# Kernel tuning notes

Measured on AMD Instinct MI355X. Metric: run time of the kernel, lower is better.

The kernel has to match this reference:

```python
import jax, jax.numpy as jnp
import numpy as np
import math

B, S, H = 2, 2048, 2048
NH, NKV, HD = 16, 4, 128


def _rope_tables(seq_len, head_dim):
    # Standard RoPE: freqs over half dim, duplicated to full head_dim.
    inv_freq = 1.0 / (10000.0 ** (np.arange(0, head_dim, 2, dtype=np.float32) / head_dim))
    t = np.arange(seq_len, dtype=np.float32)
    freqs = np.outer(t, inv_freq)  # [S, HD/2]
    emb = np.concatenate([freqs, freqs], axis=-1)  # [S, HD]
    return jnp.asarray(np.cos(emb)), jnp.asarray(np.sin(emb))


def setup_inputs() -> dict:
    key = jax.random.key(0)
    k1, k2, k3, k4 = jax.random.split(key, 4)
    cos, sin = _rope_tables(S, HD)
    return {
        "x": jax.random.normal(k1, (B, S, H), dtype=jnp.float32),
        "cos": cos,
        "sin": sin,
        "Wq": jax.random.normal(k2, (H, NH * HD), dtype=jnp.float32) * (1.0 / math.sqrt(H)),
        "Wkv": jax.random.normal(k3, (H, 2 * NKV * HD), dtype=jnp.float32) * (1.0 / math.sqrt(H)),
        "Wo": jax.random.normal(k4, (NH * HD, H), dtype=jnp.float32) * (1.0 / math.sqrt(NH * HD)),
    }


def _rotate_half(x):
    x1, x2 = jnp.split(x, 2, axis=-1)
    return jnp.concatenate([-x2, x1], axis=-1)


def _apply_rotary(x, cos, sin):
    # x: [B, S, nheads, HD]; cos/sin: [S, HD]
    c = cos[None, :, None, :]
    s = sin[None, :, None, :]
    return x * c + _rotate_half(x) * s


def reference(x, cos, sin, Wq, Wkv, Wo):
    b, s, _ = x.shape
    q = (x @ Wq).reshape(b, s, NH, HD)
    kv = x @ Wkv
    k, v = jnp.split(kv, [NKV * HD], axis=-1)
    k = k.reshape(b, s, NKV, HD)
    v = v.reshape(b, s, NKV, HD)
    q = _apply_rotary(q, cos, sin)
    k = _apply_rotary(k, cos, sin)
    # to [B, heads, S, HD]
    q = jnp.transpose(q, (0, 2, 1, 3))
    k = jnp.transpose(k, (0, 2, 1, 3))
    v = jnp.transpose(v, (0, 2, 1, 3))
    # GQA: repeat K/V heads
    rep = NH // NKV
    k = jnp.repeat(k, rep, axis=1)
    v = jnp.repeat(v, rep, axis=1)
    scale = jnp.asarray(1.0 / math.sqrt(HD), dtype=x.dtype)
    scores = jnp.einsum('bhqd,bhkd->bhqk', q * scale, k)  # [B, NH, S, S]
    causal = jnp.tril(jnp.ones((s, s), dtype=jnp.bool_))
    scores = jnp.where(causal, scores, jnp.asarray(-jnp.inf, scores.dtype))
    attn = jax.nn.softmax(scores, axis=-1)
    out = jnp.einsum('bhqk,bhkd->bhqd', attn, v)
    out = jnp.transpose(out, (0, 2, 1, 3)).reshape(b, s, NH * HD)
    return out @ Wo
```

## Files before the change

kernel.cpp:

```cpp
#include <hip/hip_runtime.h>
#include <math.h>

#define NB 2
#define SEQ 2048
#define HDIM 2048
#define NHD 16
#define NKVH 4
#define HEADD 128
#define MROWS (NB*SEQ)
#define NQCOLS (NHD*HEADD)
#define QKVCOLS 3072

typedef unsigned short ushortT;
typedef __attribute__((ext_vector_type(8))) short short8;
typedef __attribute__((ext_vector_type(4))) float floatx4;
typedef __attribute__((ext_vector_type(4))) unsigned short ushort4v;

__device__ __forceinline__ ushortT f2bf(float f) {
  union { float f; unsigned int u; } v; v.f = f;
  unsigned int r = v.u + 0x7FFFu + ((v.u >> 16) & 1u);
  return (ushortT)(r >> 16);
}
__device__ __forceinline__ float bf2f(ushortT u) {
  union { unsigned int u; float f; } v; v.u = ((unsigned int)u) << 16;
  return v.f;
}

__device__ __forceinline__ unsigned int cvt_pk_bf16(float lo, float hi) {
  unsigned int r;
  asm("v_cvt_pk_bf16_f32 %0, %1, %2" : "=v"(r) : "v"(lo), "v"(hi));
  return r;
}

__device__ __forceinline__ void gload16(const ushortT* g, ushortT* l) {
  __builtin_amdgcn_global_load_lds(
      (const __attribute__((address_space(1))) void*)g,
      (__attribute__((address_space(3))) void*)l, 16, 0, 0);
}

__global__ __launch_bounds__(256) void cast_bf16_kernel(
    const float* __restrict__ in, ushortT* __restrict__ out, int n4) {
  int i = blockIdx.x * 256 + threadIdx.x;
  if (i >= n4) return;
  float4 v = ((const float4*)in)[i];
  ushort4v o;
  o.x = f2bf(v.x); o.y = f2bf(v.y); o.z = f2bf(v.z); o.w = f2bf(v.w);
  ((ushort4v*)out)[i] = o;
}

__global__ __launch_bounds__(256) void transpose_cast_kernel(
    const float* __restrict__ in, ushortT* __restrict__ out, int R, int C) {
  __shared__ ushortT tile[32][33];
  int c0 = blockIdx.x * 32, r0 = blockIdx.y * 32;
  int tx = threadIdx.x & 31, ty = threadIdx.x >> 5;
#pragma unroll
  for (int i = 0; i < 4; ++i)
    tile[ty + i*8][tx] = f2bf(in[(size_t)(r0 + ty + i*8) * C + c0 + tx]);
  __syncthreads();
#pragma unroll
  for (int i = 0; i < 4; ++i)
    out[(size_t)(c0 + ty + i*8) * R + r0 + tx] = tile[tx][ty + i*8];
}

__global__ __launch_bounds__(256) void gemm_bt_kernel(
    const ushortT* __restrict__ A, const ushortT* __restrict__ Bt,
    void* __restrict__ C, int M, int N, int K, int c_fp32) {
  __shared__ __align__(16) ushortT lA[128 * 64];
  __shared__ __align__(16) ushortT lB[128 * 64];
  const int m0 = blockIdx.y * 128;
  const int n0 = blockIdx.x * 128;
  const int tid = threadIdx.x;
  const int wave = tid >> 6, lane = tid & 63;
  const int g = lane >> 4, l15 = lane & 15;
  const int wm = (wave >> 1) * 64, wn = (wave & 1) * 64;
  const int sw = l15 & 7;

  floatx4 acc[4][4] = {};

  for (int kt = 0; kt < K; kt += 64) {
    __syncthreads();
#pragma unroll
    for (int i = 0; i < 4; ++i) {
      int s = i * 256 + tid;
      int r = s >> 3, j = s & 7;
      int col8 = j ^ (r & 7);
      gload16(A  + (size_t)(m0 + r) * K + kt + col8 * 8, lA + s * 8);
      gload16(Bt + (size_t)(n0 + r) * K + kt + col8 * 8, lB + s * 8);
    }
    __syncthreads();
#pragma unroll
    for (int ks = 0; ks < 2; ++ks) {
      short8 af[4], bfv[4];
#pragma unroll
      for (int t = 0; t < 4; ++t) {
        af[t]  = *(const short8*)(lA + (wm + t * 16 + l15) * 64 + ((ks * 4 + g) ^ sw) * 8);
        bfv[t] = *(const short8*)(lB + (wn + t * 16 + l15) * 64 + ((ks * 4 + g) ^ sw) * 8);
      }
#pragma unroll
      for (int mt = 0; mt < 4; ++mt)
#pragma unroll
        for (int nt = 0; nt < 4; ++nt)
          acc[mt][nt] = __builtin_amdgcn_mfma_f32_16x16x32_bf16(
              af[mt], bfv[nt], acc[mt][nt], 0, 0, 0);
    }
  }

#pragma unroll
  for (int mt = 0; mt < 4; ++mt)
#pragma unroll
    for (int nt = 0; nt < 4; ++nt)
#pragma unroll
      for (int r = 0; r < 4; ++r) {
        int row = m0 + wm + mt * 16 + g * 4 + r;
        int col = n0 + wn + nt * 16 + l15;
        float v = acc[mt][nt][r];
        if (c_fp32) ((float*)C)[(size_t)row * N + col] = v;
        else ((ushortT*)C)[(size_t)row * N + col] = f2bf(v);
      }
}

__global__ __launch_bounds__(256) void rope_q_kernel(
    const ushortT* __restrict__ QKVtmp, const float* __restrict__ cosT,
    const float* __restrict__ sinT, ushortT* __restrict__ Qr) {
  int idx = blockIdx.x * 256 + threadIdx.x;
  int d = idx & 63;
  int t = idx >> 6;
  int h = t & (NHD - 1);
  int bs = t >> 4;
  int s = bs & (SEQ - 1);
  int b = bs >> 11;
  float c = cosT[s * HEADD + d], sn = sinT[s * HEADD + d];
  float q1 = bf2f(QKVtmp[(size_t)bs * QKVCOLS + h * HEADD + d]);
  float q2 = bf2f(QKVtmp[(size_t)bs * QKVCOLS + h * HEADD + d + 64]);
  size_t o = ((size_t)(b * NHD + h) * SEQ + s) * HEADD + d;
  Qr[o]      = f2bf(q1 * c - q2 * sn);
  Qr[o + 64] = f2bf(q2 * c + q1 * sn);
}

__global__ __launch_bounds__(256) void rope_k_kernel(
    const ushortT* __restrict__ QKVtmp, const float* __restrict__ cosT,
    const float* __restrict__ sinT, ushortT* __restrict__ Kr) {
  int idx = blockIdx.x * 256 + threadIdx.x;
  int d = idx & 63;
  int t = idx >> 6;
  int kvh = t & (NKVH - 1);
  int bs = t >> 2;
  int s = bs & (SEQ - 1);
  int b = bs >> 11;
  float c = cosT[s * HEADD + d], sn = sinT[s * HEADD + d];
  float k1 = bf2f(QKVtmp[(size_t)bs * QKVCOLS + 2048 + kvh * HEADD + d]);
  float k2 = bf2f(QKVtmp[(size_t)bs * QKVCOLS + 2048 + kvh * HEADD + d + 64]);
  size_t o = ((size_t)(b * NKVH + kvh) * SEQ + s) * HEADD + d;
  Kr[o]      = f2bf(k1 * c - k2 * sn);
  Kr[o + 64] = f2bf(k2 * c + k1 * sn);
}

__global__ __launch_bounds__(256) void v_relayout_kernel(
    const ushortT* __restrict__ QKVtmp, ushortT* __restrict__ Vt) {
  __shared__ ushortT tile[32][33];
  int bk = blockIdx.z;
  int b = bk >> 2, kvh = bk & 3;
  int s0 = blockIdx.x * 32, d0 = blockIdx.y * 32;
  int tx = threadIdx.x & 31, ty = threadIdx.x >> 5;
#pragma unroll
  for (int i = 0; i < 4; ++i) {
    int s = s0 + ty + i * 8;
    tile[ty + i * 8][tx] =
        QKVtmp[(size_t)(b * SEQ + s) * QKVCOLS + 2560 + kvh * HEADD + d0 + tx];
  }
  __syncthreads();
#pragma unroll
  for (int i = 0; i < 4; ++i) {
    int d = d0 + ty + i * 8;
    Vt[((size_t)bk * HEADD + d) * SEQ + s0 + tx] = tile[tx][ty + i * 8];
  }
}

__global__ __launch_bounds__(256) void attn_kernel(
    const ushortT* __restrict__ Q,
    const ushortT* __restrict__ Kg,
    const ushortT* __restrict__ Vg,
    ushortT* __restrict__ Oa) {
  __shared__ __align__(16) ushortT lK[2][64 * 128];
  __shared__ __align__(16) ushortT lV[2][128 * 64];
  __shared__ __align__(16) ushortT lP[4 * 16 * 64];

  const int tid = threadIdx.x;
  const int w = tid >> 6, lane = tid & 63;
  const int g = lane >> 4, l15 = lane & 15;
  const int sw = l15 & 7;
  const int bh = blockIdx.x;
  const int b = bh >> 4, h = bh & 15;
  const int kvh = h >> 2;
  const int yi = blockIdx.y;
  const int qiA = 31 - yi;
  const int qiB = yi;
  const int nA = qiA + 1, nB = qiB + 1;

  const float SC = 0.08838834764831845f * 1.4426950408889634f;
  const float THR = 8.0f / SC;

  const ushortT* kbase = Kg + ((size_t)(b * NKVH + kvh)) * SEQ * HEADD;
  const ushortT* vbase = Vg + ((size_t)(b * NKVH + kvh)) * HEADD * SEQ;
  ushortT* pw = lP + w * 16 * 64;

  const int qwA = (qiA << 6) + w * 16;
  const int qwB = (qiB << 6) + w * 16;

  short8 qfA[4], qfB[4];
  {
    const ushortT* qpA = Q + (((size_t)(b * NHD + h)) * SEQ + qwA + l15) * HEADD + g * 8;
    const ushortT* qpB = Q + (((size_t)(b * NHD + h)) * SEQ + qwB + l15) * HEADD + g * 8;
#pragma unroll
    for (int ks = 0; ks < 4; ++ks) {
      qfA[ks] = *(const short8*)(qpA + ks * 32);
      qfB[ks] = *(const short8*)(qpB + ks * 32);
    }
  }

  floatx4 o[8] = {};
  float m_s = -INFINITY;
  float l_s = 0.f;

  auto stage = [&](int kt, int buf) {
#pragma unroll
    for (int ii = 0; ii < 4; ++ii) {
      int s = ii * 256 + tid;
      int r = s >> 4, j = (s & 15) ^ (r & 7);
      gload16(kbase + (size_t)(kt * 64 + r) * HEADD + j * 8, lK[buf] + s * 8);
    }
#pragma unroll
    for (int ii = 0; ii < 4; ++ii) {
      int s = ii * 256 + tid;
      int r = s >> 3, j = (s & 7) ^ (r & 7);
      gload16(vbase + (size_t)r * SEQ + kt * 64 + j * 8, lV[buf] + s * 8);
    }
  };

  auto compute = [&](const short8 (&qf)[4], int qw, int kt, int cur) {
    const int rel = qw - kt * 64;

    floatx4 sc4[4] = {};
    __builtin_amdgcn_s_setprio(1);
#pragma unroll
    for (int nt = 0; nt < 4; ++nt) {
      if (nt * 16 > rel + 15) continue;
#pragma unroll
      for (int ks = 0; ks < 4; ++ks) {
        short8 kf = *(const short8*)(lK[cur] + (nt * 16 + l15) * 128 + ((ks * 4 + g) ^ sw) * 8);
        sc4[nt] = __builtin_amdgcn_mfma_f32_16x16x32_bf16(kf, qf[ks], sc4[nt], 0, 0, 0);
      }
    }
    __builtin_amdgcn_s_setprio(0);

    const bool needmask = (kt * 64 + 63) > qw;
    float ps[4][4];
    float mx = -INFINITY;
#pragma unroll
    for (int nt = 0; nt < 4; ++nt)
#pragma unroll
      for (int r = 0; r < 4; ++r) {
        float v = sc4[nt][r];
        if (needmask) {
          int kg = kt * 64 + nt * 16 + g * 4 + r;
          if (kg > qw + l15) v = -INFINITY;
        }
        ps[nt][r] = v;
        mx = fmaxf(mx, v);
      }
    mx = fmaxf(mx, __shfl_xor(mx, 16));
    mx = fmaxf(mx, __shfl_xor(mx, 32));

    float mn;
    if (__all(mx <= m_s + THR)) {
      mn = m_s;
    } else {
      mn = fmaxf(m_s, mx);
      float alpha = __builtin_amdgcn_exp2f((m_s - mn) * SC);
      l_s *= alpha;
#pragma unroll
      for (int dt = 0; dt < 8; ++dt)
#pragma unroll
        for (int r = 0; r < 4; ++r) o[dt][r] *= alpha;
      m_s = mn;
    }
    const float mnSC = mn * SC;

    float rs = 0.f;
#pragma unroll
    for (int nt = 0; nt < 4; ++nt) {
      float e[4];
#pragma unroll
      for (int r = 0; r < 4; ++r) {
        e[r] = __builtin_amdgcn_exp2f(__builtin_fmaf(ps[nt][r], SC, -mnSC));
        rs += e[r];
      }
      uint2 pk;
      pk.x = cvt_pk_bf16(e[0], e[1]);
      pk.y = cvt_pk_bf16(e[2], e[3]);
      *(uint2*)(pw + l15 * 64 + (((nt * 2 + (g >> 1)) ^ sw) * 8 + (g & 1) * 4)) = pk;
    }
    rs += __shfl_xor(rs, 16);
    rs += __shfl_xor(rs, 32);
    l_s += rs;

    __builtin_amdgcn_s_setprio(1);
#pragma unroll
    for (int ks = 0; ks < 2; ++ks) {
      if (kt * 64 + ks * 32 > qw + 15) continue;
      short8 bp = *(const short8*)(pw + l15 * 64 + ((ks * 4 + g) ^ sw) * 8);
#pragma unroll
      for (int dt = 0; dt < 8; ++dt) {
        short8 vf = *(const short8*)(lV[cur] + (dt * 16 + l15) * 64 + ((ks * 4 + g) ^ sw) * 8);
        o[dt] = __builtin_amdgcn_mfma_f32_16x16x32_bf16(vf, bp, o[dt], 0, 0, 0);
      }
    }
    __builtin_amdgcn_s_setprio(0);
  };

  auto epilogue = [&](int qw) {
    float inv = 1.f / l_s;
    int qg = qw + l15;
#pragma unroll
    for (int dt = 0; dt < 8; ++dt) {
      uint2 ov;
      ov.x = cvt_pk_bf16(o[dt][0] * inv, o[dt][1] * inv);
      ov.y = cvt_pk_bf16(o[dt][2] * inv, o[dt][3] * inv);
      *(uint2*)(Oa + (size_t)(b * SEQ + qg) * NQCOLS + h * HEADD + dt * 16 + g * 4) = ov;
    }
  };

  stage(0, 0);
  asm volatile("s_waitcnt vmcnt(0)" ::: "memory");
  __builtin_amdgcn_s_barrier();

  for (int kt = 0; kt < nA; ++kt) {
    const int cur = kt & 1;
    if (kt + 1 < nA) stage(kt + 1, cur ^ 1);
    else             stage(0, cur ^ 1);
    compute(qfA, qwA, kt, cur);
    asm volatile("s_waitcnt vmcnt(0)" ::: "memory");
    __builtin_amdgcn_s_barrier();
  }
  epilogue(qwA);
#pragma unroll
  for (int dt = 0; dt < 8; ++dt) o[dt] = floatx4{0.f, 0.f, 0.f, 0.f};
  m_s = -INFINITY; l_s = 0.f;

  for (int kt = 0; kt < nB; ++kt) {
    const int cur = (nA + kt) & 1;
    if (kt + 1 < nB) stage(kt + 1, cur ^ 1);
    compute(qfB, qwB, kt, cur);
    asm volatile("s_waitcnt vmcnt(0)" ::: "memory");
    __builtin_amdgcn_s_barrier();
  }
  epilogue(qwB);
}

extern "C" void kernel_launch(void* const* d_in, const int* in_sizes, int n_in,
                              void* d_out, int out_size, void* d_ws, size_t ws_size,
                              hipStream_t stream) {
  const float* x    = (const float*)d_in[0];
  const float* cosT = (const float*)d_in[1];
  const float* sinT = (const float*)d_in[2];
  const float* Wq   = (const float*)d_in[3];
  const float* Wkv  = (const float*)d_in[4];
  const float* Wo   = (const float*)d_in[5];

  char* ws = (char*)d_ws;
  ushortT* x_bf   = (ushortT*)(ws + 0);
  ushortT* Wqkvt  = (ushortT*)(ws + 16777216);
  ushortT* Wot    = (ushortT*)(ws + 29360128);
  ushortT* QKVtmp = (ushortT*)(ws + 37748736);
  ushortT* Qr     = (ushortT*)(ws + 62914560);
  ushortT* Kr     = (ushortT*)(ws + 79691776);
  ushortT* Vt     = (ushortT*)(ws + 83886080);
  ushortT* Oattn  = QKVtmp;

  cast_bf16_kernel<<<8192, 256, 0, stream>>>(x, x_bf, (MROWS * HDIM) / 4);
  transpose_cast_kernel<<<dim3(64, 64), 256, 0, stream>>>(Wq, Wqkvt, HDIM, NQCOLS);
  transpose_cast_kernel<<<dim3(32, 64), 256, 0, stream>>>(Wkv, Wqkvt + 2048 * 2048, HDIM, 1024);
  transpose_cast_kernel<<<dim3(64, 64), 256, 0, stream>>>(Wo, Wot, NQCOLS, HDIM);

  gemm_bt_kernel<<<dim3(24, 32), 256, 0, stream>>>(x_bf, Wqkvt, QKVtmp, MROWS, QKVCOLS, HDIM, 0);

  rope_q_kernel<<<16384, 256, 0, stream>>>(QKVtmp, cosT, sinT, Qr);
  rope_k_kernel<<<4096, 256, 0, stream>>>(QKVtmp, cosT, sinT, Kr);
  v_relayout_kernel<<<dim3(64, 4, 8), 256, 0, stream>>>(QKVtmp, Vt);

  attn_kernel<<<dim3(32, 16), 256, 0, stream>>>(Qr, Kr, Vt, Oattn);

  gemm_bt_kernel<<<dim3(16, 32), 256, 0, stream>>>(Oattn, Wot, d_out, MROWS, HDIM, NQCOLS, 1);
}
```

Measured before the change: 339.5 us.

## Replace GEMM with 256x256 double-buffered tile kernel interleaving prefetch and MFMA

Replaces the 128x128 single-buffered GEMM with a 512-thread kernel that computes 256x256 output tiles. It double-buffers LDS and issues the next k-tile's global-to-LDS loads in quarters between MFMA groups, raising MFMA priority with s_setprio. The larger tile is meant to improve data reuse and hide load latency. In exchange it uses about 128KB of LDS per block, and the grids shrink to 192 and 128 blocks, which may leave many of the 256 CUs idle.

Result: slower. 346.7 us (+2.1%).

```diff
diff --git a/kernel.cpp b/kernel.cpp
--- a/kernel.cpp
+++ b/kernel.cpp
@@ -62,51 +62,100 @@
     out[(size_t)(c0 + ty + i*8) * R + r0 + tx] = tile[tx][ty + i*8];
 }
 
-__global__ __launch_bounds__(256) void gemm_bt_kernel(
+__global__ __launch_bounds__(512, 2) void gemm256_kernel(
     const ushortT* __restrict__ A, const ushortT* __restrict__ Bt,
     void* __restrict__ C, int M, int N, int K, int c_fp32) {
-  __shared__ __align__(16) ushortT lA[128 * 64];
-  __shared__ __align__(16) ushortT lB[128 * 64];
-  const int m0 = blockIdx.y * 128;
-  const int n0 = blockIdx.x * 128;
+  __shared__ __align__(16) ushortT lA[2][256 * 64];
+  __shared__ __align__(16) ushortT lB[2][256 * 64];
+  const int m0 = blockIdx.y * 256;
+  const int n0 = blockIdx.x * 256;
   const int tid = threadIdx.x;
-  const int wave = tid >> 6, lane = tid & 63;
+  const int lane = tid & 63;
+  const int wave = tid >> 6;
   const int g = lane >> 4, l15 = lane & 15;
-  const int wm = (wave >> 1) * 64, wn = (wave & 1) * 64;
+  const int wr = wave >> 2, wc = wave & 3;
+  const int wm = wr * 128, wn = wc * 64;
   const int sw = l15 & 7;
 
-  floatx4 acc[4][4] = {};
-
-  for (int kt = 0; kt < K; kt += 64) {
-    __syncthreads();
-#pragma unroll
-    for (int i = 0; i < 4; ++i) {
-      int s = i * 256 + tid;
+  floatx4 acc[8][4] = {};
+
+  auto stageA = [&](int kt, int buf, int ha) {
+#pragma unroll
+    for (int i = 0; i < 2; ++i) {
+      int s = i * 512 + tid;
       int r = s >> 3, j = s & 7;
       int col8 = j ^ (r & 7);
-      gload16(A  + (size_t)(m0 + r) * K + kt + col8 * 8, lA + s * 8);
-      gload16(Bt + (size_t)(n0 + r) * K + kt + col8 * 8, lB + s * 8);
-    }
-    __syncthreads();
-#pragma unroll
-    for (int ks = 0; ks < 2; ++ks) {
-      short8 af[4], bfv[4];
-#pragma unroll
-      for (int t = 0; t < 4; ++t) {
-        af[t]  = *(const short8*)(lA + (wm + t * 16 + l15) * 64 + ((ks * 4 + g) ^ sw) * 8);
-        bfv[t] = *(const short8*)(lB + (wn + t * 16 + l15) * 64 + ((ks * 4 + g) ^ sw) * 8);
-      }
+      gload16(A + (size_t)(m0 + ha * 128 + r) * K + kt + col8 * 8,
+              lA[buf] + ha * 128 * 64 + s * 8);
+    }
+  };
+  auto stageB = [&](int kt, int buf, int hb) {
+#pragma unroll
+    for (int i = 0; i < 2; ++i) {
+      int s = i * 512 + tid;
+      int r = s >> 3, j = s & 7;
+      int col8 = j ^ (r & 7);
+      gload16(Bt + (size_t)(n0 + hb * 128 + r) * K + kt + col8 * 8,
+              lB[buf] + hb * 128 * 64 + s * 8);
+    }
+  };
+
+  stageA(0, 0, 0); stageA(0, 0, 1); stageB(0, 0, 0); stageB(0, 0, 1);
+  asm volatile("s_waitcnt vmcnt(0)" ::: "memory");
+  __builtin_amdgcn_s_barrier();
+
+  const int NT = K >> 6;
+  for (int t = 0; t < NT; ++t) {
+    const int c = t & 1;
+    const int ktn = (t + 1) << 6;
+    const bool more = (t + 1) < NT;
+    const ushortT* la = lA[c];
+    const ushortT* lb = lB[c];
+
+    short8 af[4][2], bf[2][2];
+#pragma unroll
+    for (int q = 0; q < 4; ++q) {
+      const int mh = q >> 1, nh = q & 1;
+      __builtin_amdgcn_s_barrier();
+      if (nh == 0) {
+#pragma unroll
+        for (int mt = 0; mt < 4; ++mt) {
+          int row = wm + mh * 64 + mt * 16 + l15;
+#pragma unroll
+          for (int ks = 0; ks < 2; ++ks)
+            af[mt][ks] = *(const short8*)(la + row * 64 + ((ks * 4 + g) ^ sw) * 8);
+        }
+      }
+#pragma unroll
+      for (int nt = 0; nt < 2; ++nt) {
+        int col = wn + nh * 32 + nt * 16 + l15;
+#pragma unroll
+        for (int ks = 0; ks < 2; ++ks)
+          bf[nt][ks] = *(const short8*)(lb + col * 64 + ((ks * 4 + g) ^ sw) * 8);
+      }
+      if (more) {
+        if (q == 0)      stageA(ktn, c ^ 1, 0);
+        else if (q == 1) stageA(ktn, c ^ 1, 1);
+        else if (q == 2) stageB(ktn, c ^ 1, 0);
+        else             stageB(ktn, c ^ 1, 1);
+      }
+      __builtin_amdgcn_s_setprio(1);
 #pragma unroll
       for (int mt = 0; mt < 4; ++mt)
 #pragma unroll
-        for (int nt = 0; nt < 4; ++nt)
-          acc[mt][nt] = __builtin_amdgcn_mfma_f32_16x16x32_bf16(
-              af[mt], bfv[nt], acc[mt][nt], 0, 0, 0);
-    }
-  }
-
-#pragma unroll
-  for (int mt = 0; mt < 4; ++mt)
+        for (int nt = 0; nt < 2; ++nt)
+#pragma unroll
+          for (int ks = 0; ks < 2; ++ks)
+            acc[mh * 4 + mt][nh * 2 + nt] = __builtin_amdgcn_mfma_f32_16x16x32_bf16(
+                af[mt][ks], bf[nt][ks], acc[mh * 4 + mt][nh * 2 + nt], 0, 0, 0);
+      __builtin_amdgcn_s_setprio(0);
+    }
+    asm volatile("s_waitcnt vmcnt(0)" ::: "memory");
+    __builtin_amdgcn_s_barrier();
+  }
+
+#pragma unroll
+  for (int mt = 0; mt < 8; ++mt)
 #pragma unroll
     for (int nt = 0; nt < 4; ++nt)
 #pragma unroll
@@ -382,7 +431,7 @@
   transpose_cast_kernel<<<dim3(32, 64), 256, 0, stream>>>(Wkv, Wqkvt + 2048 * 2048, HDIM, 1024);
   transpose_cast_kernel<<<dim3(64, 64), 256, 0, stream>>>(Wo, Wot, NQCOLS, HDIM);
 
-  gemm_bt_kernel<<<dim3(24, 32), 256, 0, stream>>>(x_bf, Wqkvt, QKVtmp, MROWS, QKVCOLS, HDIM, 0);
+  gemm256_kernel<<<dim3(12, 16), 512, 0, stream>>>(x_bf, Wqkvt, QKVtmp, MROWS, QKVCOLS, HDIM, 0);
 
   rope_q_kernel<<<16384, 256, 0, stream>>>(QKVtmp, cosT, sinT, Qr);
   rope_k_kernel<<<4096, 256, 0, stream>>>(QKVtmp, cosT, sinT, Kr);
@@ -390,5 +439,5 @@
 
   attn_kernel<<<dim3(32, 16), 256, 0, stream>>>(Qr, Kr, Vt, Oattn);
 
-  gemm_bt_kernel<<<dim3(16, 32), 256, 0, stream>>>(Oattn, Wot, d_out, MROWS, HDIM, NQCOLS, 1);
-}
+  gemm256_kernel<<<dim3(8, 16), 512, 0, stream>>>(Oattn, Wot, d_out, MROWS, HDIM, NQCOLS, 1);
+}
```

## Replace GEMMs with 4-stage LDS ring pipeline and merge prep kernels

Applied to the files above, without the earlier changes.

Replaces the single-buffered 128x128 GEMM with a 512-thread kernel that computes 256x256 (QKV) or 128x256 (output) tiles. A 4-deep ring of K=32 LDS buffers is filled via direct-to-LDS loads, with explicit vmcnt waits and raised MFMA priority, so global loads overlap with matrix math. The three weight transpose-cast launches become one kernel, and the Q and K RoPE kernels become one, which cuts launch overhead. The larger tiles and deeper buffering use more LDS and registers and produce fewer blocks, which may lower occupancy. Wot must now sit right after Wqkvt in the workspace, since the merged transpose writes both through one pointer.

Result: faster. 313.6 us (-7.6%).

```diff
diff --git a/kernel.cpp b/kernel.cpp
--- a/kernel.cpp
+++ b/kernel.cpp
@@ -38,6 +38,13 @@
       (__attribute__((address_space(3))) void*)l, 16, 0, 0);
 }
 
+__device__ __forceinline__ void tile_barrier() {
+  asm volatile("" ::: "memory");
+  __builtin_amdgcn_s_barrier();
+  asm volatile("" ::: "memory");
+  __builtin_amdgcn_sched_barrier(0);
+}
+
 __global__ __launch_bounds__(256) void cast_bf16_kernel(
     const float* __restrict__ in, ushortT* __restrict__ out, int n4) {
   int i = blockIdx.x * 256 + threadIdx.x;
@@ -48,111 +55,163 @@
   ((ushort4v*)out)[i] = o;
 }
 
-__global__ __launch_bounds__(256) void transpose_cast_kernel(
-    const float* __restrict__ in, ushortT* __restrict__ out, int R, int C) {
+__global__ __launch_bounds__(256) void transpose_cast3_kernel(
+    const float* __restrict__ Wq, const float* __restrict__ Wkv,
+    const float* __restrict__ Wo, ushortT* __restrict__ out) {
   __shared__ ushortT tile[32][33];
-  int c0 = blockIdx.x * 32, r0 = blockIdx.y * 32;
+  int cu0 = blockIdx.x * 32, r0 = blockIdx.y * 32;
+  const float* src; int C, c0;
+  if (cu0 < 2048)      { src = Wq;  C = 2048; c0 = cu0; }
+  else if (cu0 < 3072) { src = Wkv; C = 1024; c0 = cu0 - 2048; }
+  else                 { src = Wo;  C = 2048; c0 = cu0 - 3072; }
   int tx = threadIdx.x & 31, ty = threadIdx.x >> 5;
 #pragma unroll
   for (int i = 0; i < 4; ++i)
-    tile[ty + i*8][tx] = f2bf(in[(size_t)(r0 + ty + i*8) * C + c0 + tx]);
+    tile[ty + i*8][tx] = f2bf(src[(size_t)(r0 + ty + i*8) * C + c0 + tx]);
   __syncthreads();
 #pragma unroll
   for (int i = 0; i < 4; ++i)
-    out[(size_t)(c0 + ty + i*8) * R + r0 + tx] = tile[tx][ty + i*8];
-}
-
-__global__ __launch_bounds__(256) void gemm_bt_kernel(
+    out[(size_t)(cu0 + ty + i*8) * 2048 + r0 + tx] = tile[tx][ty + i*8];
+}
+
+template <int MH>
+__global__ __launch_bounds__(512, 2) void gemm_ring_kernel(
     const ushortT* __restrict__ A, const ushortT* __restrict__ Bt,
     void* __restrict__ C, int M, int N, int K, int c_fp32) {
-  __shared__ __align__(16) ushortT lA[128 * 64];
-  __shared__ __align__(16) ushortT lB[128 * 64];
-  const int m0 = blockIdx.y * 128;
-  const int n0 = blockIdx.x * 128;
+  constexpr int BM = 128 * MH;
+  constexpr int LPT = MH + 2;
+  __shared__ __align__(16) ushortT lA[4][BM * 32];
+  __shared__ __align__(16) ushortT lB[4][256 * 32];
+  const int m0 = blockIdx.y * BM;
+  const int n0 = blockIdx.x * 256;
   const int tid = threadIdx.x;
-  const int wave = tid >> 6, lane = tid & 63;
+  const int lane = tid & 63, wave = tid >> 6;
   const int g = lane >> 4, l15 = lane & 15;
-  const int wm = (wave >> 1) * 64, wn = (wave & 1) * 64;
-  const int sw = l15 & 7;
-
-  floatx4 acc[4][4] = {};
-
-  for (int kt = 0; kt < K; kt += 64) {
-    __syncthreads();
-#pragma unroll
-    for (int i = 0; i < 4; ++i) {
-      int s = i * 256 + tid;
-      int r = s >> 3, j = s & 7;
-      int col8 = j ^ (r & 7);
-      gload16(A  + (size_t)(m0 + r) * K + kt + col8 * 8, lA + s * 8);
-      gload16(Bt + (size_t)(n0 + r) * K + kt + col8 * 8, lB + s * 8);
-    }
-    __syncthreads();
-#pragma unroll
-    for (int ks = 0; ks < 2; ++ks) {
-      short8 af[4], bfv[4];
-#pragma unroll
-      for (int t = 0; t < 4; ++t) {
-        af[t]  = *(const short8*)(lA + (wm + t * 16 + l15) * 64 + ((ks * 4 + g) ^ sw) * 8);
-        bfv[t] = *(const short8*)(lB + (wn + t * 16 + l15) * 64 + ((ks * 4 + g) ^ sw) * 8);
-      }
+  const int wr = wave >> 2, wc = wave & 3;
+  const int wm = wr * (BM / 2), wn = wc * 64;
+
+  floatx4 acc[4 * MH][4] = {};
+
+  auto stageA = [&](int u) {
+    ushortT* dst = lA[u & 3];
+    const int kt = u << 5;
+#pragma unroll
+    for (int i = 0; i < MH; ++i) {
+      int s = i * 512 + tid;
+      int r = s >> 2, j = s & 3;
+      int jj = j ^ ((r >> 1) & 3);
+      gload16(A + (size_t)(m0 + r) * K + kt + jj * 8, dst + s * 8);
+    }
+  };
+  auto stageB = [&](int u) {
+    ushortT* dst = lB[u & 3];
+    const int kt = u << 5;
+#pragma unroll
+    for (int i = 0; i < 2; ++i) {
+      int s = i * 512 + tid;
+      int r = s >> 2, j = s & 3;
+      int jj = j ^ ((r >> 1) & 3);
+      gload16(Bt + (size_t)(n0 + r) * K + kt + jj * 8, dst + s * 8);
+    }
+  };
+
+  stageA(0); stageB(0); stageA(1); stageB(1); stageA(2); stageB(2);
+
+  const int NT = K >> 5;
+  for (int u = 0; u < NT; ++u) {
+    if constexpr (MH == 2) {
+      if (u + 2 < NT)      asm volatile("s_waitcnt vmcnt(8)" ::: "memory");
+      else if (u + 1 < NT) asm volatile("s_waitcnt vmcnt(4)" ::: "memory");
+      else                 asm volatile("s_waitcnt vmcnt(0)" ::: "memory");
+    } else {
+      if (u + 2 < NT)      asm volatile("s_waitcnt vmcnt(6)" ::: "memory");
+      else if (u + 1 < NT) asm volatile("s_waitcnt vmcnt(3)" ::: "memory");
+      else                 asm volatile("s_waitcnt vmcnt(0)" ::: "memory");
+    }
+    tile_barrier();
+
+    const ushortT* la = lA[u & 3];
+    const ushortT* lb = lB[u & 3];
+    const bool more = (u + 3) < NT;
+
+    short8 bfr[4];
+#pragma unroll
+    for (int nt = 0; nt < 4; ++nt) {
+      int col = wn + nt * 16 + l15;
+      bfr[nt] = *(const short8*)(lb + col * 32 + (g ^ ((col >> 1) & 3)) * 8);
+    }
+
+#pragma unroll
+    for (int mh = 0; mh < MH; ++mh) {
+      if (mh) tile_barrier();
+      short8 afr[4];
+#pragma unroll
+      for (int mt = 0; mt < 4; ++mt) {
+        int row = wm + mh * 64 + mt * 16 + l15;
+        afr[mt] = *(const short8*)(la + row * 32 + (g ^ ((row >> 1) & 3)) * 8);
+      }
+      if (more) {
+        if (mh == 0) stageA(u + 3);
+        if (mh == MH - 1) stageB(u + 3);
+      }
+      __builtin_amdgcn_s_setprio(1);
 #pragma unroll
       for (int mt = 0; mt < 4; ++mt)
 #pragma unroll
         for (int nt = 0; nt < 4; ++nt)
-          acc[mt][nt] = __builtin_amdgcn_mfma_f32_16x16x32_bf16(
-              af[mt], bfv[nt], acc[mt][nt], 0, 0, 0);
-    }
-  }
-
-#pragma unroll
-  for (int mt = 0; mt < 4; ++mt)
+          acc[mh * 4 + mt][nt] = __builtin_amdgcn_mfma_f32_16x16x32_bf16(
+              afr[mt], bfr[nt], acc[mh * 4 + mt][nt], 0, 0, 0);
+      __builtin_amdgcn_s_setprio(0);
+    }
+  }
+
+#pragma unroll
+  for (int fm = 0; fm < 4 * MH; ++fm)
 #pragma unroll
     for (int nt = 0; nt < 4; ++nt)
 #pragma unroll
-      for (int r = 0; r < 4; ++r) {
-        int row = m0 + wm + mt * 16 + g * 4 + r;
+      for (int r4 = 0; r4 < 4; ++r4) {
+        int row = m0 + wm + fm * 16 + g * 4 + r4;
         int col = n0 + wn + nt * 16 + l15;
-        float v = acc[mt][nt][r];
+        float v = acc[fm][nt][r4];
         if (c_fp32) ((float*)C)[(size_t)row * N + col] = v;
         else ((ushortT*)C)[(size_t)row * N + col] = f2bf(v);
       }
 }
 
-__global__ __launch_bounds__(256) void rope_q_kernel(
+__global__ __launch_bounds__(256) void rope_qk_kernel(
     const ushortT* __restrict__ QKVtmp, const float* __restrict__ cosT,
-    const float* __restrict__ sinT, ushortT* __restrict__ Qr) {
+    const float* __restrict__ sinT, ushortT* __restrict__ Qr,
+    ushortT* __restrict__ Kr) {
   int idx = blockIdx.x * 256 + threadIdx.x;
-  int d = idx & 63;
-  int t = idx >> 6;
-  int h = t & (NHD - 1);
-  int bs = t >> 4;
-  int s = bs & (SEQ - 1);
-  int b = bs >> 11;
-  float c = cosT[s * HEADD + d], sn = sinT[s * HEADD + d];
-  float q1 = bf2f(QKVtmp[(size_t)bs * QKVCOLS + h * HEADD + d]);
-  float q2 = bf2f(QKVtmp[(size_t)bs * QKVCOLS + h * HEADD + d + 64]);
-  size_t o = ((size_t)(b * NHD + h) * SEQ + s) * HEADD + d;
-  Qr[o]      = f2bf(q1 * c - q2 * sn);
-  Qr[o + 64] = f2bf(q2 * c + q1 * sn);
-}
-
-__global__ __launch_bounds__(256) void rope_k_kernel(
-    const ushortT* __restrict__ QKVtmp, const float* __restrict__ cosT,
-    const float* __restrict__ sinT, ushortT* __restrict__ Kr) {
-  int idx = blockIdx.x * 256 + threadIdx.x;
-  int d = idx & 63;
-  int t = idx >> 6;
-  int kvh = t & (NKVH - 1);
-  int bs = t >> 2;
-  int s = bs & (SEQ - 1);
-  int b = bs >> 11;
-  float c = cosT[s * HEADD + d], sn = sinT[s * HEADD + d];
-  float k1 = bf2f(QKVtmp[(size_t)bs * QKVCOLS + 2048 + kvh * HEADD + d]);
-  float k2 = bf2f(QKVtmp[(size_t)bs * QKVCOLS + 2048 + kvh * HEADD + d + 64]);
-  size_t o = ((size_t)(b * NKVH + kvh) * SEQ + s) * HEADD + d;
-  Kr[o]      = f2bf(k1 * c - k2 * sn);
-  Kr[o + 64] = f2bf(k2 * c + k1 * sn);
+  if (idx < NB * SEQ * NHD * 64) {
+    int d = idx & 63;
+    int t = idx >> 6;
+    int h = t & (NHD - 1);
+    int bs = t >> 4;
+    int s = bs & (SEQ - 1);
+    int b = bs >> 11;
+    float c = cosT[s * HEADD + d], sn = sinT[s * HEADD + d];
+    float q1 = bf2f(QKVtmp[(size_t)bs * QKVCOLS + h * HEADD + d]);
+    float q2 = bf2f(QKVtmp[(size_t)bs * QKVCOLS + h * HEADD + d + 64]);
+    size_t o = ((size_t)(b * NHD + h) * SEQ + s) * HEADD + d;
+    Qr[o]      = f2bf(q1 * c - q2 * sn);
+    Qr[o + 64] = f2bf(q2 * c + q1 * sn);
+  } else {
+    int k = idx - NB * SEQ * NHD * 64;
+    int d = k & 63;
+    int t = k >> 6;
+    int kvh = t & (NKVH - 1);
+    int bs = t >> 2;
+    int s = bs & (SEQ - 1);
+    int b = bs >> 11;
+    float c = cosT[s * HEADD + d], sn = sinT[s * HEADD + d];
+    float k1 = bf2f(QKVtmp[(size_t)bs * QKVCOLS + 2048 + kvh * HEADD + d]);
+    float k2 = bf2f(QKVtmp[(size_t)bs * QKVCOLS + 2048 + kvh * HEADD + d + 64]);
+    size_t o = ((size_t)(b * NKVH + kvh) * SEQ + s) * HEADD + d;
+    Kr[o]      = f2bf(k1 * c - k2 * sn);
+    Kr[o + 64] = f2bf(k2 * c + k1 * sn);
+  }
 }
 
 __global__ __launch_bounds__(256) void v_relayout_kernel(
@@ -378,17 +437,16 @@
   ushortT* Oattn  = QKVtmp;
 
   cast_bf16_kernel<<<8192, 256, 0, stream>>>(x, x_bf, (MROWS * HDIM) / 4);
-  transpose_cast_kernel<<<dim3(64, 64), 256, 0, stream>>>(Wq, Wqkvt, HDIM, NQCOLS);
-  transpose_cast_kernel<<<dim3(32, 64), 256, 0, stream>>>(Wkv, Wqkvt + 2048 * 2048, HDIM, 1024);
-  transpose_cast_kernel<<<dim3(64, 64), 256, 0, stream>>>(Wo, Wot, NQCOLS, HDIM);
-
-  gemm_bt_kernel<<<dim3(24, 32), 256, 0, stream>>>(x_bf, Wqkvt, QKVtmp, MROWS, QKVCOLS, HDIM, 0);
-
-  rope_q_kernel<<<16384, 256, 0, stream>>>(QKVtmp, cosT, sinT, Qr);
-  rope_k_kernel<<<4096, 256, 0, stream>>>(QKVtmp, cosT, sinT, Kr);
+  transpose_cast3_kernel<<<dim3(160, 64), 256, 0, stream>>>(Wq, Wkv, Wo, Wqkvt);
+
+  gemm_ring_kernel<2><<<dim3(12, 16), 512, 0, stream>>>(x_bf, Wqkvt, QKVtmp,
+                                                        MROWS, QKVCOLS, HDIM, 0);
+
+  rope_qk_kernel<<<20480, 256, 0, stream>>>(QKVtmp, cosT, sinT, Qr, Kr);
   v_relayout_kernel<<<dim3(64, 4, 8), 256, 0, stream>>>(QKVtmp, Vt);
 
   attn_kernel<<<dim3(32, 16), 256, 0, stream>>>(Qr, Kr, Vt, Oattn);
 
-  gemm_bt_kernel<<<dim3(16, 32), 256, 0, stream>>>(Oattn, Wot, d_out, MROWS, HDIM, NQCOLS, 1);
-}
+  gemm_ring_kernel<1><<<dim3(8, 32), 512, 0, stream>>>(Oattn, Wot, d_out,
+                                                       MROWS, HDIM, NQCOLS, 1);
+}
```
